# Kernel tuning notes

Measured on AMD Instinct MI355X. Metric: run time of the kernel, lower is better.

## Reference

```python
import jax, jax.numpy as jnp
import numpy as np
import math

D_MODEL = 1024
N_HEADS = 16
D_K = D_MODEL // N_HEADS
B, S = 4, 2048


def setup_inputs() -> dict:
    key = jax.random.key(0)
    ks = jax.random.split(key, 11)
    sc = 1.0 / math.sqrt(D_MODEL)
    inp = {
        'q': jax.random.normal(ks[0], (B, S, D_MODEL), jnp.float32),
        'k': jax.random.normal(ks[1], (B, S, D_MODEL), jnp.float32),
        'v': jax.random.normal(ks[2], (B, S, D_MODEL), jnp.float32),
        'mask': jnp.tril(jnp.ones((S, S), jnp.int32))[None, None],  # [1,1,S,S] causal
        'wq': jax.random.normal(ks[3], (D_MODEL, D_MODEL), jnp.float32) * sc,
        'bq': jnp.zeros((D_MODEL,), jnp.float32),
        'wk': jax.random.normal(ks[4], (D_MODEL, D_MODEL), jnp.float32) * sc,
        'bk': jnp.zeros((D_MODEL,), jnp.float32),
        'wv': jax.random.normal(ks[5], (D_MODEL, D_MODEL), jnp.float32) * sc,
        'bv': jnp.zeros((D_MODEL,), jnp.float32),
        'wo': jax.random.normal(ks[6], (D_MODEL, D_MODEL), jnp.float32) * sc,
        'bo': jnp.zeros((D_MODEL,), jnp.float32),
    }
    return inp


def reference(q, k, v, mask, wq, bq, wk, bk, wv, bv, wo, bo):
    b = q.shape[0]
    # projections: [B,S,D] -> [B,H,S,d_k]
    def split_heads(x):
        return x.reshape(b, -1, N_HEADS, D_K).transpose(0, 2, 1, 3)
    qh = split_heads(q @ wq + bq)
    kh = split_heads(k @ wk + bk)
    vh = split_heads(v @ wv + bv)
    # scores: [B,H,S,S]
    scores = jnp.einsum('bhqd,bhkd->bhqk', qh, kh) / math.sqrt(D_K)
    scores = jnp.where(mask == 0, jnp.float32(-1e9), scores)
    attn = jax.nn.softmax(scores, axis=-1)
    # dropout is identity in eval mode (deterministic reference)
    ctx = jnp.einsum('bhqk,bhkd->bhqd', attn, vh)
    ctx = ctx.transpose(0, 2, 1, 3).reshape(b, -1, D_MODEL)
    return ctx @ wo + bo
```

## Files before the change

kernel.cpp:

```cpp
#include <hip/hip_runtime.h>
#include <hip/hip_bf16.h>

#define D_MODEL 1024
#define N_HEADS 16
#define DK 64
#define SEQ 2048
#define BATCH 4

typedef __attribute__((ext_vector_type(4))) float   f32v4;
typedef __attribute__((ext_vector_type(16))) float  f32v16;
typedef __attribute__((ext_vector_type(8))) __bf16  bf16x8;
typedef __attribute__((ext_vector_type(8))) unsigned short u16v8;
typedef __attribute__((ext_vector_type(4))) unsigned short u16v4;
typedef __attribute__((ext_vector_type(4))) unsigned int   u32v4;

#define QSCALE 0.18033688011112042f
#define SMBIAS 12.0f

__device__ __forceinline__ int swz(int byte) {
    return byte ^ (((byte >> 7) & 7) << 4);
}

__device__ __forceinline__ unsigned short bfb(float f) {
    return __builtin_bit_cast(unsigned short, (__bf16)f);
}
__device__ __forceinline__ float bff(unsigned short u) {
    return (float)__builtin_bit_cast(__bf16, u);
}

__device__ __forceinline__ f32v4 mfma16(bf16x8 a, bf16x8 b, f32v4 c) {
    return __builtin_amdgcn_mfma_f32_16x16x32_bf16(a, b, c, 0, 0, 0);
}
__device__ __forceinline__ f32v16 mfma32(bf16x8 a, bf16x8 b, f32v16 c) {
    return __builtin_amdgcn_mfma_f32_32x32x16_bf16(a, b, c, 0, 0, 0);
}

#define GL2LDS16(gp, lp) \
    __builtin_amdgcn_global_load_lds((__attribute__((address_space(1))) const void*)(gp), \
                                     (__attribute__((address_space(3))) void*)(lp), 16, 0, 0)

#define VMWAIT(N) asm volatile("s_waitcnt vmcnt(" #N ")" ::: "memory")
#define LGKM0()   asm volatile("s_waitcnt lgkmcnt(0)" ::: "memory")

__global__ __launch_bounds__(256) void wtrans_kernel(const float* wq, const float* wk,
                                                     const float* wv, const float* wo,
                                                     unsigned short* wt) {
    __shared__ unsigned short ts[64][65];
    int bid = blockIdx.x;
    int mat = bid >> 8;
    int tile = bid & 255;
    int kb = (tile >> 4) * 64;
    int nb = (tile & 15) * 64;
    const float* W = (mat == 0) ? wq : (mat == 1) ? wk : (mat == 2) ? wv : wo;
    unsigned short* out = wt + (size_t)mat * D_MODEL * D_MODEL;
    int t = threadIdx.x;
#pragma unroll
    for (int p = 0; p < 4; ++p) {
        int row = p * 16 + (t >> 4);
        int c0 = (t & 15) * 4;
        f32v4 v = *(const f32v4*)(W + (size_t)(kb + row) * D_MODEL + nb + c0);
#pragma unroll
        for (int j = 0; j < 4; ++j) ts[row][c0 + j] = bfb(v[j]);
    }
    __syncthreads();
#pragma unroll
    for (int p = 0; p < 2; ++p) {
        int n = p * 32 + (t >> 3);
        int k0 = (t & 7) * 8;
        u16v8 o;
#pragma unroll
        for (int j = 0; j < 8; ++j) o[j] = ts[k0 + j][n];
        *(u16v8*)(out + (size_t)(nb + n) * D_MODEL + kb + k0) = o;
    }
}

__global__ __launch_bounds__(512, 1) void qkv_kernel(const float* __restrict__ qin,
                                                     const float* __restrict__ kin,
                                                     const float* __restrict__ vin,
                                                     const unsigned short* __restrict__ WT,
                                                     const float* __restrict__ bq,
                                                     const float* __restrict__ bk,
                                                     const float* __restrict__ bv,
                                                     unsigned short* __restrict__ Qh,
                                                     unsigned short* __restrict__ Kh,
                                                     unsigned short* __restrict__ Vtp) {
    __shared__ unsigned short lds[3][(256 + 128) * 64];
    int bid0 = blockIdx.x;
    int mat = bid0 >> 8;
    int bidl = bid0 & 255;
    const float* Af = (mat == 0) ? qin : (mat == 1) ? kin : vin;
    const unsigned short* Wt = WT + (size_t)mat * D_MODEL * D_MODEL;
    const float* bias = (mat == 0) ? bq : (mat == 1) ? bk : bv;
    bool vmode = (mat == 2);
    float osc = (mat == 0) ? QSCALE : 1.0f;

    int xcd = bidl & 7, blki = bidl >> 3;
    int mb = (xcd * 4 + (blki >> 3)) * 256;
    int nb = (blki & 7) * 128;
    int tid = threadIdx.x;
    int lane = tid & 63, wid = tid >> 6;
    int l15 = lane & 15, g = lane >> 4;
    int r7 = lane >> 3, slot = lane & 7;
    int wr = wid >> 1, wc = wid & 1;
    int ssrc = (slot ^ r7) * 8;

    f32v4 acc[4][4] = {};

    char* p0 = (char*)lds[0];
    char* p1 = (char*)lds[1];
    char* p2 = (char*)lds[2];

    int arow = tid >> 4;
    int acol = (tid & 15) * 4;
    f32v4 a_stg[8];

    auto stage_issue = [&](char* buf, int k0) {
#pragma unroll
        for (int j = 0; j < 8; ++j)
            a_stg[j] = *(const f32v4*)(Af + (size_t)(mb + j * 32 + arow) * D_MODEL + k0 + acol);
#pragma unroll
        for (int ii = 0; ii < 2; ++ii) {
            int c = ii * 8 + wid;
            GL2LDS16(Wt + (size_t)(nb + c * 8 + r7) * D_MODEL + k0 + ssrc, buf + 32768 + c * 1024);
        }
    };
    auto stage_write = [&](char* buf) {
#pragma unroll
        for (int j = 0; j < 8; ++j) {
            u16v4 o;
#pragma unroll
            for (int e = 0; e < 4; ++e) o[e] = bfb(a_stg[j][e]);
            int row = j * 32 + arow;
            *(u16v4*)(buf + swz(row * 128 + (tid & 15) * 8)) = o;
        }
    };
    auto fragA = [&](char* buf, int row, int kk) -> bf16x8 {
        int sl = (kk * 4 + g) ^ (row & 7);
        return *(bf16x8*)(buf + row * 128 + sl * 16);
    };
    auto fragB = [&](char* buf, int row, int kk) -> bf16x8 {
        int sl = (kk * 4 + g) ^ (row & 7);
        return *(bf16x8*)(buf + 32768 + row * 128 + sl * 16);
    };

    stage_issue(p0, 0);
    stage_write(p0);
    stage_issue(p1, 64);
    stage_write(p1);
    VMWAIT(2);
    LGKM0();
    __builtin_amdgcn_s_barrier();
    __builtin_amdgcn_sched_barrier(0);

    for (int t = 0; t < 16; ++t) {
        if (t + 2 < 16) stage_issue(p2, (t + 2) * 64);
#pragma unroll
        for (int kk = 0; kk < 2; ++kk) {
            bf16x8 fa[4], fb[4];
            if (!vmode) {
#pragma unroll
                for (int mt = 0; mt < 4; ++mt) fa[mt] = fragA(p0, wr * 64 + mt * 16 + l15, kk);
#pragma unroll
                for (int nt = 0; nt < 4; ++nt) fb[nt] = fragB(p0, wc * 64 + nt * 16 + l15, kk);
            } else {
#pragma unroll
                for (int xx = 0; xx < 4; ++xx) fa[xx] = fragB(p0, wc * 64 + xx * 16 + l15, kk);
#pragma unroll
                for (int yy = 0; yy < 4; ++yy) fb[yy] = fragA(p0, wr * 64 + yy * 16 + l15, kk);
            }
            __builtin_amdgcn_s_setprio(1);
#pragma unroll
            for (int a = 0; a < 4; ++a)
#pragma unroll
                for (int b = 0; b < 4; ++b)
                    acc[a][b] = mfma16(fa[a], fb[b], acc[a][b]);
            __builtin_amdgcn_s_setprio(0);
        }
        if (t + 2 < 16) stage_write(p2);
        if (t < 14) { VMWAIT(2); } else { VMWAIT(0); }
        LGKM0();
        __builtin_amdgcn_s_barrier();
        __builtin_amdgcn_sched_barrier(0);
        char* tp = p0; p0 = p1; p1 = p2; p2 = tp;
    }

    if (!vmode) {
        unsigned short* out = (mat == 0) ? Qh : Kh;
#pragma unroll
        for (int nt = 0; nt < 4; ++nt) {
            int n = nb + wc * 64 + nt * 16 + l15;
            float bvv = bias[n];
#pragma unroll
            for (int mt = 0; mt < 4; ++mt) {
#pragma unroll
                for (int r = 0; r < 4; ++r) {
                    int m = mb + wr * 64 + mt * 16 + 4 * g + r;
                    float val = (acc[mt][nt][r] + bvv) * osc;
                    int bb = m >> 11, ss = m & 2047, hh = n >> 6, dd = n & 63;
                    out[(((size_t)(bb * N_HEADS + hh)) * SEQ + ss) * DK + dd] = bfb(val);
                }
            }
        }
    } else {
#pragma unroll
        for (int xx = 0; xx < 4; ++xx) {
#pragma unroll
            for (int r = 0; r < 4; ++r) {
                int n = nb + wc * 64 + xx * 16 + 4 * g + r;
                float bvv = bias[n];
                int hh = n >> 6, dd = n & 63;
#pragma unroll
                for (int yy = 0; yy < 4; ++yy) {
                    int tok = mb + wr * 64 + yy * 16 + l15;
                    int bb = tok >> 11, ss = tok & 2047;
                    float val = acc[xx][yy][r] + bvv;
                    Vtp[((size_t)(bb * N_HEADS + hh) * DK + dd) * SEQ + ss] = bfb(val);
                }
            }
        }
    }
}

__global__ __launch_bounds__(512, 1) void gemmo_kernel(const unsigned short* __restrict__ A,
                                                       const unsigned short* __restrict__ Wt,
                                                       const float* __restrict__ bias, float* Cptr) {
    __shared__ unsigned short lds[3][(256 + 128) * 64];
    int bid0 = blockIdx.x;
    int xcd = bid0 & 7, blki = bid0 >> 3;
    int mb = (xcd * 4 + (blki >> 3)) * 256;
    int nb = (blki & 7) * 128;
    int tid = threadIdx.x;
    int lane = tid & 63, wid = tid >> 6;
    int l15 = lane & 15, g = lane >> 4;
    int r7 = lane >> 3, slot = lane & 7;
    int wr = wid >> 1, wc = wid & 1;
    int ssrc = (slot ^ r7) * 8;

    f32v4 acc[4][4] = {};
    char* p0 = (char*)lds[0];
    char* p1 = (char*)lds[1];
    char* p2 = (char*)lds[2];

    auto stage = [&](char* buf, int k0) {
#pragma unroll
        for (int ii = 0; ii < 4; ++ii) {
            int c = ii * 8 + wid;
            GL2LDS16(A + (size_t)(mb + c * 8 + r7) * D_MODEL + k0 + ssrc, buf + c * 1024);
        }
#pragma unroll
        for (int ii = 0; ii < 2; ++ii) {
            int c = ii * 8 + wid;
            GL2LDS16(Wt + (size_t)(nb + c * 8 + r7) * D_MODEL + k0 + ssrc, buf + 32768 + c * 1024);
        }
    };
    auto fragA = [&](char* buf, int row, int kk) -> bf16x8 {
        int sl = (kk * 4 + g) ^ (row & 7);
        return *(bf16x8*)(buf + row * 128 + sl * 16);
    };
    auto fragB = [&](char* buf, int row, int kk) -> bf16x8 {
        int sl = (kk * 4 + g) ^ (row & 7);
        return *(bf16x8*)(buf + 32768 + row * 128 + sl * 16);
    };

    stage(p0, 0);
    stage(p1, 64);
    VMWAIT(6);
    __builtin_amdgcn_s_barrier();
    __builtin_amdgcn_sched_barrier(0);

    for (int t = 0; t < 16; ++t) {
        if (t + 2 < 16) stage(p2, (t + 2) * 64);
#pragma unroll
        for (int kk = 0; kk < 2; ++kk) {
            bf16x8 fa[4], fb[4];
#pragma unroll
            for (int mt = 0; mt < 4; ++mt) fa[mt] = fragA(p0, wr * 64 + mt * 16 + l15, kk);
#pragma unroll
            for (int nt = 0; nt < 4; ++nt) fb[nt] = fragB(p0, wc * 64 + nt * 16 + l15, kk);
            __builtin_amdgcn_s_setprio(1);
#pragma unroll
            for (int a = 0; a < 4; ++a)
#pragma unroll
                for (int b = 0; b < 4; ++b)
                    acc[a][b] = mfma16(fa[a], fb[b], acc[a][b]);
            __builtin_amdgcn_s_setprio(0);
        }
        if (t < 14) { VMWAIT(6); } else { VMWAIT(0); }
        __builtin_amdgcn_s_barrier();
        __builtin_amdgcn_sched_barrier(0);
        char* tp = p0; p0 = p1; p1 = p2; p2 = tp;
    }

#pragma unroll
    for (int nt = 0; nt < 4; ++nt) {
        int n = nb + wc * 64 + nt * 16 + l15;
        float bv = bias[n];
#pragma unroll
        for (int mt = 0; mt < 4; ++mt) {
#pragma unroll
            for (int r = 0; r < 4; ++r) {
                int m = mb + wr * 64 + mt * 16 + 4 * g + r;
                Cptr[(size_t)m * D_MODEL + n] = acc[mt][nt][r] + bv;
            }
        }
    }
}

__global__ __launch_bounds__(256, 4) void attn_kernel(const unsigned short* Qh, const unsigned short* Kh,
                                                      const unsigned short* Vt, unsigned short* ctxp) {
    __shared__ unsigned short k_lds[2][64 * 64];
    __shared__ unsigned short v_lds[2][64 * 64];
    int bid = blockIdx.x;
    int jq = bid >> 8, x = (bid >> 6) & 3;
    int tile = (jq == 0) ? (15 - x) : (jq == 1) ? (8 + x) : (jq == 2) ? (7 - x) : x;
    int bh = bid & 63;
    int bb = bh >> 4, hh = bh & 15;
    int tid = threadIdx.x;
    int wid = tid >> 6, lane = tid & 63;
    int l31 = lane & 31, hi = lane >> 5;
    int qw0 = tile * 128 + wid * 32;
    int qg = qw0 + l31;
    const unsigned short* Qb = Qh + (size_t)bh * SEQ * DK;
    const unsigned short* Kb = Kh + (size_t)bh * SEQ * DK;
    const unsigned short* Vb = Vt + (size_t)bh * DK * SEQ;

    bf16x8 qf[4];
#pragma unroll
    for (int ks = 0; ks < 4; ++ks)
        qf[ks] = *(const bf16x8*)(Qb + (size_t)qg * DK + ks * 16 + hi * 8);

    f32v16 o0 = {}, o1 = {};
    float lsum = 0.f;
    int n_kt = 2 * tile + 2;

    const int klane = 16 * (lane ^ (lane >> 3));
    const int vlane = 16 * ((lane & 7) ^ (lane >> 3));
    auto stage = [&](int bufi, int kg) {
        const char* kb0 = (const char*)(Kb + (size_t)kg * DK);
        const char* vb0 = (const char*)Vb + (size_t)kg * 2;
#pragma unroll
        for (int jj = 0; jj < 2; ++jj) {
            int base = wid * 2048 + jj * 1024;
            GL2LDS16(kb0 + base + klane, (char*)k_lds[bufi] + base);
            GL2LDS16(vb0 + (size_t)(wid * 16 + jj * 8 + (lane >> 3)) * (SEQ * 2) + vlane,
                     (char*)v_lds[bufi] + base);
        }
    };

#define PACK2(a, b) (((unsigned)bfb(b) << 16) | (unsigned)bfb(a))
#define PVSTEP(tt, r0, ks, vl)                                                          \
    {                                                                                   \
        unsigned x0 = PACK2(tt[r0 + 0], tt[r0 + 1]);                                    \
        unsigned x1 = PACK2(tt[r0 + 2], tt[r0 + 3]);                                    \
        unsigned x2 = PACK2(tt[r0 + 4], tt[r0 + 5]);                                    \
        unsigned x3 = PACK2(tt[r0 + 6], tt[r0 + 7]);                                    \
        asm volatile("v_permlane32_swap_b32 %0, %1" : "+v"(x0), "+v"(x2));              \
        asm volatile("v_permlane32_swap_b32 %0, %1" : "+v"(x1), "+v"(x3));              \
        u32v4 w;                                                                        \
        w[0] = x0;  w[1] = x1;  w[2] = x2;  w[3] = x3;                                  \
        bf16x8 paf = __builtin_bit_cast(bf16x8, w);                                     \
        bf16x8 vf0 = *(bf16x8*)((char*)(vl) + swz(l31 * 128 + ks * 32 + hi * 16));      \
        bf16x8 vf1 = *(bf16x8*)((char*)(vl) + swz((32 + l31) * 128 + ks * 32 + hi * 16)); \
        o0 = mfma32(paf, vf0, o0);                                                      \
        o1 = mfma32(paf, vf1, o1);                                                      \
    }

    auto compute_tile = [&](int ktb, const unsigned short* kl, const unsigned short* vl) {
        if (ktb > qw0 + 31) return;
        f32v16 t0 = {}, t1 = {};
        __builtin_amdgcn_s_setprio(1);
#pragma unroll
        for (int ks = 0; ks < 4; ++ks) {
            bf16x8 kf0 = *(bf16x8*)((char*)kl + swz(l31 * 128 + ks * 32 + hi * 16));
            bf16x8 kf1 = *(bf16x8*)((char*)kl + swz((32 + l31) * 128 + ks * 32 + hi * 16));
            t0 = mfma32(kf0, qf[ks], t0);
            t1 = mfma32(kf1, qf[ks], t1);
        }
        __builtin_amdgcn_s_setprio(0);
        if (ktb + 63 > qw0) {
#pragma unroll
            for (int r = 0; r < 16; ++r) {
                int off = (r & 3) + 8 * (r >> 2) + 4 * hi;
                if (ktb + off > qg) t0[r] = -1e30f;
                if (ktb + 32 + off > qg) t1[r] = -1e30f;
            }
        }
#pragma unroll
        for (int r = 0; r < 16; ++r) {
            t0[r] = __builtin_amdgcn_exp2f(t0[r] - SMBIAS);
            t1[r] = __builtin_amdgcn_exp2f(t1[r] - SMBIAS);
            lsum += t0[r] + t1[r];
        }
        __builtin_amdgcn_s_setprio(1);
        PVSTEP(t0, 0, 0, vl)
        PVSTEP(t0, 8, 1, vl)
        PVSTEP(t1, 0, 2, vl)
        PVSTEP(t1, 8, 3, vl)
        __builtin_amdgcn_s_setprio(0);
    };

    stage(0, 0);
    __syncthreads();
    int buf = 0;
    for (int kt = 0; kt < n_kt; ++kt) {
        if (kt + 1 < n_kt) stage(buf ^ 1, (kt + 1) * 64);
        compute_tile(kt * 64, k_lds[buf], v_lds[buf]);
        __syncthreads();
        buf ^= 1;
    }

    float lt = lsum + __shfl_xor(lsum, 32);
    float rinv = 1.f / lt;
#pragma unroll
    for (int r = 0; r < 16; ++r) {
        int off = (r & 3) + 8 * (r >> 2) + 4 * hi;
        float rr = __shfl(rinv, off);
        int qq = qw0 + off;
        size_t base = ((size_t)(bb * SEQ + qq)) * D_MODEL + hh * DK;
        ctxp[base + l31] = bfb(o0[r] * rr);
        ctxp[base + 32 + l31] = bfb(o1[r] * rr);
    }
#undef PVSTEP
#undef PACK2
}

extern "C" void kernel_launch(void* const* d_in, const int* in_sizes, int n_in,
                              void* d_out, int out_size, void* d_ws, size_t ws_size,
                              hipStream_t stream) {
    const float* q  = (const float*)d_in[0];
    const float* k  = (const float*)d_in[1];
    const float* v  = (const float*)d_in[2];
    const float* wq = (const float*)d_in[4];
    const float* bq = (const float*)d_in[5];
    const float* wk = (const float*)d_in[6];
    const float* bk = (const float*)d_in[7];
    const float* wv = (const float*)d_in[8];
    const float* bv = (const float*)d_in[9];
    const float* wo = (const float*)d_in[10];
    const float* bo = (const float*)d_in[11];

    unsigned short* ws  = (unsigned short*)d_ws;
    const size_t M8 = (size_t)8 * 1024 * 1024;
    unsigned short* Qh = ws;
    unsigned short* Kh = ws + M8;
    unsigned short* Vt = ws + 2 * M8;
    unsigned short* X  = ws + 3 * M8;
    unsigned short* WT = ws + 4 * M8;
    const size_t MM = (size_t)D_MODEL * D_MODEL;

    wtrans_kernel<<<dim3(1024), dim3(256), 0, stream>>>(wq, wk, wv, wo, WT);
    qkv_kernel<<<dim3(768), dim3(512), 0, stream>>>(q, k, v, WT, bq, bk, bv, Qh, Kh, Vt);
    attn_kernel<<<dim3(1024), dim3(256), 0, stream>>>(Qh, Kh, Vt, X);
    gemmo_kernel<<<dim3(256), dim3(512), 0, stream>>>(X, WT + 3 * MM, bo, (float*)d_out);
}
```

Baseline: 164.5 us.

## Deepen A-operand register prefetch by one stage in projection GEMM pipeline

Splits the staging step into separate A global-load, A LDS-write and B direct-to-LDS DMA steps. A tiles are now loaded into registers one iteration earlier (k+3), so their global latency is hidden behind a full MFMA iteration before conversion and LDS write. The vmcnt waits are retuned to match, and the last barrier is skipped. The risk is a mis-set wait count, which could race on the LDS buffers, and the prefetch registers stay live across the MFMA loop, which adds register pressure.

Result: slower. 172.4 us (+4.8%).

```diff
diff --git a/kernel.cpp b/kernel.cpp
--- a/kernel.cpp
+++ b/kernel.cpp
@@ -114,17 +114,19 @@
     int acol = (tid & 15) * 4;
     f32v4 a_stg[8];
 
-    auto stage_issue = [&](char* buf, int k0) {
-#pragma unroll
-        for (int j = 0; j < 8; ++j)
-            a_stg[j] = *(const f32v4*)(Af + (size_t)(mb + j * 32 + arow) * D_MODEL + k0 + acol);
+    auto dmaB = [&](char* buf, int k0) {
 #pragma unroll
         for (int ii = 0; ii < 2; ++ii) {
             int c = ii * 8 + wid;
             GL2LDS16(Wt + (size_t)(nb + c * 8 + r7) * D_MODEL + k0 + ssrc, buf + 32768 + c * 1024);
         }
     };
-    auto stage_write = [&](char* buf) {
+    auto issueA = [&](int k0) {
+#pragma unroll
+        for (int j = 0; j < 8; ++j)
+            a_stg[j] = *(const f32v4*)(Af + (size_t)(mb + j * 32 + arow) * D_MODEL + k0 + acol);
+    };
+    auto writeA = [&](char* buf) {
 #pragma unroll
         for (int j = 0; j < 8; ++j) {
             u16v4 o;
@@ -143,17 +145,24 @@
         return *(bf16x8*)(buf + 32768 + row * 128 + sl * 16);
     };
 
-    stage_issue(p0, 0);
-    stage_write(p0);
-    stage_issue(p1, 64);
-    stage_write(p1);
-    VMWAIT(2);
+    dmaB(p0, 0);
+    issueA(0);
+    writeA(p0);
+    dmaB(p1, 64);
+    issueA(64);
+    writeA(p1);
+    issueA(128);
+    VMWAIT(8);
     LGKM0();
     __builtin_amdgcn_s_barrier();
     __builtin_amdgcn_sched_barrier(0);
 
     for (int t = 0; t < 16; ++t) {
-        if (t + 2 < 16) stage_issue(p2, (t + 2) * 64);
+        if (t < 14) {
+            writeA(p2);
+            dmaB(p2, (t + 2) * 64);
+        }
+        if (t < 13) issueA((t + 3) * 64);
 #pragma unroll
         for (int kk = 0; kk < 2; ++kk) {
             bf16x8 fa[4], fb[4];
@@ -176,11 +185,14 @@
                     acc[a][b] = mfma16(fa[a], fb[b], acc[a][b]);
             __builtin_amdgcn_s_setprio(0);
         }
-        if (t + 2 < 16) stage_write(p2);
-        if (t < 14) { VMWAIT(2); } else { VMWAIT(0); }
-        LGKM0();
-        __builtin_amdgcn_s_barrier();
-        __builtin_amdgcn_sched_barrier(0);
+        if (t < 15) {
+            if (t < 13)      { VMWAIT(10); }
+            else if (t == 13){ VMWAIT(2); }
+            else             { VMWAIT(0); }
+            LGKM0();
+            __builtin_amdgcn_s_barrier();
+            __builtin_amdgcn_sched_barrier(0);
+        }
         char* tp = p0; p0 = p1; p1 = p2; p2 = tp;
     }
 
```
